# Performance work log

Hardware: AMD Instinct MI355X
Metric: run time of the kernel (lower is better)

Reference implementation:

```python
import jax, jax.numpy as jnp
import numpy as np

B, T, C, H = 2, 1024, 768, 12
D = C // H
HID = 4 * C
EPS_YAT = 1e-6
EPS_LN = 1e-6


def yat_dense(x, kernel, bias, alpha):
    # scale = (sqrt(n_out)/log(1+n_out))**alpha
    y = x @ kernel
    dist = (jnp.sum(x * x, axis=-1, keepdims=True)
            + jnp.sum(kernel * kernel, axis=0) - 2.0 * y)
    y = (y * y) / (dist + EPS_YAT)
    if bias is not None:
        y = y + bias
    n = kernel.shape[1]
    scale = (jnp.sqrt(jnp.float32(n)) / jnp.log1p(jnp.float32(n))) ** alpha
    return y * scale


def layernorm(x, scale):
    mu = jnp.mean(x, axis=-1, keepdims=True)
    var = jnp.mean((x - mu) ** 2, axis=-1, keepdims=True)
    return (x - mu) * jax.lax.rsqrt(var + EPS_LN) * scale


def rope_table(seq_len, dim):
    freqs = jnp.exp(jnp.arange(0, dim, 2, dtype=jnp.float32)
                    * (-jnp.log(10000.0) / dim))
    angles = jnp.arange(seq_len, dtype=jnp.float32)[:, None] * freqs[None, :]
    return jnp.concatenate([jnp.cos(angles), jnp.sin(angles)], axis=-1)  # [T, D]


def block_forward(x, mask, p):
    Bc, Tc, Cc = x.shape
    h = layernorm(x, p['ln1_scale'])
    qkv = yat_dense(h, p['w_qkv'], p['b_qkv'], p['a_qkv'])  # [B,T,3C]
    qkv = qkv.reshape(Bc, Tc, 3, H, D)
    q, k, v = qkv[:, :, 0], qkv[:, :, 1], qkv[:, :, 2]      # [B,T,H,D]
    rope = rope_table(Tc, D)[:, None, :]                     # [T,1,D]
    q = q * rope
    k = k * rope
    scale = 1.0 / jnp.sqrt(jnp.float32(D))
    attn = jnp.einsum('bihd,bjhd->bhij', q, k) * scale       # [B,H,T,T]
    attn = jnp.where(mask, attn, jnp.finfo(attn.dtype).min)
    attn = jax.nn.softmax(attn, axis=-1)
    o = jnp.einsum('bhij,bjhd->bihd', attn, v).reshape(Bc, Tc, Cc)
    o = yat_dense(o, p['w_ao'], p['b_ao'], p['a_ao'])
    x = x + o
    h = layernorm(x, p['ln2_scale'])
    gate = yat_dense(h, p['w_fc'], p['b_fc'], p['a_fc'])
    u = yat_dense(h, p['w_gate'], p['b_gate'], p['a_gate'])
    u = jax.nn.gelu(u) * gate
    u = yat_dense(u, p['w_proj'], p['b_proj'], p['a_proj'])
    return x + u


def setup_inputs() -> dict:
    key = jax.random.key(0)
    ks = jax.random.split(key, 8)
    x = jax.random.normal(ks[0], (B, T, C), dtype=jnp.float32)
    mask = jnp.tril(jnp.ones((T, T), dtype=bool))[None, None]  # causal [1,1,T,T]
    w = lambda k, shp: 0.02 * jax.random.normal(k, shp, dtype=jnp.float32)
    return {
        'x': x, 'mask': mask,
        'ln1_scale': jnp.ones((C,), jnp.float32),
        'w_qkv': w(ks[1], (C, 3 * C)), 'b_qkv': jnp.zeros((3 * C,), jnp.float32),
        'a_qkv': jnp.ones((1,), jnp.float32),
        'w_ao': w(ks[2], (C, C)), 'b_ao': jnp.zeros((C,), jnp.float32),
        'a_ao': jnp.ones((1,), jnp.float32),
        'ln2_scale': jnp.ones((C,), jnp.float32),
        'w_fc': w(ks[3], (C, HID)), 'b_fc': jnp.zeros((HID,), jnp.float32),
        'a_fc': jnp.ones((1,), jnp.float32),
        'w_gate': w(ks[4], (C, HID)), 'b_gate': jnp.zeros((HID,), jnp.float32),
        'a_gate': jnp.ones((1,), jnp.float32),
        'w_proj': w(ks[5], (HID, C)), 'b_proj': jnp.zeros((C,), jnp.float32),
        'a_proj': jnp.ones((1,), jnp.float32),
    }


def reference(x, mask, ln1_scale, w_qkv, b_qkv, a_qkv, w_ao, b_ao, a_ao,
              ln2_scale, w_fc, b_fc, a_fc, w_gate, b_gate, a_gate,
              w_proj, b_proj, a_proj):
    p = dict(ln1_scale=ln1_scale, w_qkv=w_qkv, b_qkv=b_qkv, a_qkv=a_qkv,
             w_ao=w_ao, b_ao=b_ao, a_ao=a_ao, ln2_scale=ln2_scale,
             w_fc=w_fc, b_fc=b_fc, a_fc=a_fc, w_gate=w_gate, b_gate=b_gate,
             a_gate=a_gate, w_proj=w_proj, b_proj=b_proj, a_proj=a_proj)
    return block_forward(x, mask, p)
```

## Files before the change

### kernel.cpp

```cpp
#include <hip/hip_runtime.h>
#include <cstdint>

#define DEVFN static __device__ __forceinline__

typedef __bf16 bf16x8 __attribute__((ext_vector_type(8)));
typedef float f32x4 __attribute__((ext_vector_type(4)));
typedef float f32x16 __attribute__((ext_vector_type(16)));
typedef unsigned short us4 __attribute__((ext_vector_type(4)));

DEVFN unsigned short f2bf(float f) {
  unsigned u = __float_as_uint(f);
  u += 0x7fffu + ((u >> 16) & 1u);
  return (unsigned short)(u >> 16);
}
DEVFN float bf2f(unsigned short h) { return __uint_as_float(((unsigned)h) << 16); }
DEVFN void async16(const void* g, void* l) {
  __builtin_amdgcn_global_load_lds((__attribute__((address_space(1))) const void*)g,
                                   (__attribute__((address_space(3))) void*)l, 16, 0, 0);
}
DEVFN float gelu_t(float u) {
  float z = 0.7978845608028654f * (u + 0.044715f * u * u * u);
  float zc = fminf(fmaxf(z, -15.f), 15.f);
  float e = __expf(2.f * zc);
  return u * __fdividef(e, e + 1.f);
}
DEVFN int xcd_swizzle(int lin, int total) {
  return (lin & 7) * (total >> 3) + (lin >> 3);
}
DEVFN int row32(int r, int lhalf) { return (r & 3) + 8 * (r >> 2) + 4 * lhalf; }

struct PrepArgs {
  float* rope;
  const float* W[5]; unsigned short* Wt[5]; float* cn[5];
  int N[5]; int off[6];
  const float* x; const float* g1s; unsigned short* h1; float* hrow1;
};
__global__ __launch_bounds__(256) void k_prep(PrepArgs a) {
  __shared__ float tile[32][33];
  __shared__ float part[8][32];
  __shared__ float red[12];
  const int bid = blockIdx.x, tid = threadIdx.x;
  if (bid < 256) {
    int g = bid * 256 + tid;
    int t = g >> 6, dd = g & 63, i = dd & 31;
    float fr = __expf(-0.2878231366242558f * (float)i);
    float ang = (float)t * fr;
    a.rope[g] = (dd < 32) ? cosf(ang) : sinf(ang);
  } else if (bid < 9472) {
    int lin = bid - 256;
    int e = 0;
    while (lin >= a.off[e + 1]) ++e;
    int local = lin - a.off[e];
    const int N = a.N[e];
    int nbx = N >> 5;
    int tn = local % nbx, tk = local / nbx;
    const float* W = a.W[e];
    unsigned short* Wt = a.Wt[e];
    float* cn = a.cn[e];
    const int K = (e == 4) ? 3072 : 768;
    int tx = tid & 31, ty = tid >> 5;
    float acc = 0.f;
    #pragma unroll
    for (int j = 0; j < 4; ++j) {
      int r = ty + j * 8;
      float v = W[(long)(tk * 32 + r) * N + tn * 32 + tx];
      tile[r][tx] = v;
      acc += v * v;
    }
    part[ty][tx] = acc;
    __syncthreads();
    #pragma unroll
    for (int j = 0; j < 4; ++j) {
      int rr = ty + j * 8;
      Wt[(long)(tn * 32 + rr) * K + tk * 32 + tx] = f2bf(tile[tx][rr]);
    }
    if (ty == 0) {
      float s = part[0][tx];
      #pragma unroll
      for (int jj = 1; jj < 8; ++jj) s += part[jj][tx];
      atomicAdd(&cn[tn * 32 + tx], s);
    }
  } else {
    int row = bid - 9472;
    const float* xr = a.x + (long)row * 768;
    float v0 = xr[tid], v1 = xr[tid + 256], v2 = xr[tid + 512];
    float s = v0 + v1 + v2;
    float ss = v0 * v0 + v1 * v1 + v2 * v2;
    #pragma unroll
    for (int o = 32; o; o >>= 1) { s += __shfl_xor(s, o); ss += __shfl_xor(ss, o); }
    int wv = tid >> 6;
    if ((tid & 63) == 0) { red[wv] = s; red[wv + 4] = ss; }
    __syncthreads();
    s = red[0] + red[1] + red[2] + red[3];
    ss = red[4] + red[5] + red[6] + red[7];
    float mu = s * (1.f / 768.f);
    float var = ss * (1.f / 768.f) - mu * mu;
    float rs = rsqrtf(var + 1e-6f);
    float h0 = (v0 - mu) * rs * a.g1s[tid];
    float h1 = (v1 - mu) * rs * a.g1s[tid + 256];
    float h2 = (v2 - mu) * rs * a.g1s[tid + 512];
    unsigned short* hr = a.h1 + (long)row * 768;
    hr[tid] = f2bf(h0); hr[tid + 256] = f2bf(h1); hr[tid + 512] = f2bf(h2);
    float p = h0 * h0 + h1 * h1 + h2 * h2;
    #pragma unroll
    for (int o = 32; o; o >>= 1) p += __shfl_xor(p, o);
    if ((tid & 63) == 0) red[8 + wv] = p;
    __syncthreads();
    if (tid == 0) a.hrow1[row] = red[8] + red[9] + red[10] + red[11];
  }
}

__global__ __launch_bounds__(256) void k_ln(const float* __restrict__ x,
    const float* __restrict__ g, unsigned short* __restrict__ h, float* __restrict__ row2) {
  int row = blockIdx.x, tid = threadIdx.x;
  const float* xr = x + (long)row * 768;
  float v0 = xr[tid], v1 = xr[tid + 256], v2 = xr[tid + 512];
  float s = v0 + v1 + v2;
  float ss = v0 * v0 + v1 * v1 + v2 * v2;
  #pragma unroll
  for (int o = 32; o; o >>= 1) { s += __shfl_xor(s, o); ss += __shfl_xor(ss, o); }
  __shared__ float red[12];
  int wv = tid >> 6;
  if ((tid & 63) == 0) { red[wv] = s; red[wv + 4] = ss; }
  __syncthreads();
  s = red[0] + red[1] + red[2] + red[3];
  ss = red[4] + red[5] + red[6] + red[7];
  float mu = s * (1.f / 768.f);
  float var = ss * (1.f / 768.f) - mu * mu;
  float rs = rsqrtf(var + 1e-6f);
  float h0 = (v0 - mu) * rs * g[tid];
  float h1 = (v1 - mu) * rs * g[tid + 256];
  float h2 = (v2 - mu) * rs * g[tid + 512];
  unsigned short* hr = h + (long)row * 768;
  hr[tid] = f2bf(h0); hr[tid + 256] = f2bf(h1); hr[tid + 512] = f2bf(h2);
  float p = h0 * h0 + h1 * h1 + h2 * h2;
  #pragma unroll
  for (int o = 32; o; o >>= 1) p += __shfl_xor(p, o);
  if ((tid & 63) == 0) red[8 + wv] = p;
  __syncthreads();
  if (tid == 0) row2[row] = red[8] + red[9] + red[10] + red[11];
}

constexpr int M_QKV = 0, M_AO = 1;

struct GemmArgs {
  const unsigned short* A; const unsigned short* Bt;
  const float* arow2; const float* wcol2; const float* bias; const float* alpha;
  int N; int ks;
  const float* rope;
  unsigned short* qo; unsigned short* ko; unsigned short* vo;
  const float* xf; float* xo;
};

template <int MODE, int NI, int NBM, int NBN>
__global__ __launch_bounds__(256, 4) void k_gemm(GemmArgs p) {
  __shared__ __align__(16) unsigned short As[3][2048];
  __shared__ __align__(16) unsigned short Bs[3][4096];
  const int tid = threadIdx.x, wave = tid >> 6, lane = tid & 63;
  const int quad = lane >> 4, l = lane & 15;
  constexpr int TOTAL = NBM * NBN;
  const int g = xcd_swizzle(blockIdx.x, TOTAL);
  const int bm = (g % NBM) * 64;
  const int bn = (g / NBM) * 128;
  const int ks = p.ks;
  const int wm = (wave & 1) * 32, wn = (wave >> 1) * 64;
  const f32x4 fzero = {0.f, 0.f, 0.f, 0.f};
  f32x4 acc[2][4];
  #pragma unroll
  for (int i = 0; i < 2; ++i)
    #pragma unroll
    for (int j = 0; j < 4; ++j) acc[i][j] = fzero;
  const int sw = (l >> 1) & 3;

  auto stage = [&](int s, int k0) {
    {
      int ci = tid;
      int r = ci >> 2;
      int c = (ci & 3) ^ ((r >> 1) & 3);
      async16(p.A + (long)(bm + r) * ks + k0 + c * 8, &As[s][ci * 8]);
    }
    #pragma unroll
    for (int it = 0; it < 2; ++it) {
      int ci = tid + it * 256;
      int r = ci >> 2;
      int c = (ci & 3) ^ ((r >> 1) & 3);
      async16(p.Bt + (long)(bn + r) * ks + k0 + c * 8, &Bs[s][ci * 8]);
    }
  };
  auto compute = [&](int s) {
    bf16x8 af[2], bfv[4];
    #pragma unroll
    for (int mi = 0; mi < 2; ++mi)
      af[mi] = *(const bf16x8*)&As[s][(wm + mi * 16 + l) * 32 + ((quad ^ sw) * 8)];
    #pragma unroll
    for (int ni = 0; ni < 4; ++ni)
      bfv[ni] = *(const bf16x8*)&Bs[s][(wn + ni * 16 + l) * 32 + ((quad ^ sw) * 8)];
    #pragma unroll
    for (int mi = 0; mi < 2; ++mi)
      #pragma unroll
      for (int ni = 0; ni < 4; ++ni)
        acc[mi][ni] = __builtin_amdgcn_mfma_f32_16x16x32_bf16(af[mi], bfv[ni], acc[mi][ni], 0, 0, 0);
  };
  auto iter = [&](int s, int i) {
    if (i + 1 >= NI) { asm volatile("s_waitcnt vmcnt(0)" ::: "memory"); }
    else             { asm volatile("s_waitcnt vmcnt(3)" ::: "memory"); }
    __builtin_amdgcn_s_barrier();
    asm volatile("" ::: "memory");
    if (i + 2 < NI) stage(s == 0 ? 2 : s - 1, (i + 2) * 32);
    compute(s);
  };

  stage(0, 0);
  stage(1, 32);
  int i = 0;
  while (i < NI) {
    iter(0, i); ++i;
    iter(1, i); ++i;
    iter(2, i); ++i;
  }

  const float al = p.alpha[0];
  const float nn = (float)p.N;
  const float ys = powf(sqrtf(nn) / log1pf(nn), al);
  #pragma unroll
  for (int ni = 0; ni < 4; ++ni) {
    const int j = bn + wn + ni * 16 + l;
    const float w2 = p.wcol2[j];
    const float bj = p.bias[j];
    int s3 = 0, hh = 0, dd = 0;
    if constexpr (MODE == M_QKV) { s3 = j / 768; int rem = j - s3 * 768; hh = rem >> 6; dd = rem & 63; }
    #pragma unroll
    for (int mi = 0; mi < 2; ++mi) {
      const int i0 = bm + wm + mi * 16 + quad * 4;
      float vv[4];
      #pragma unroll
      for (int rg = 0; rg < 4; ++rg) {
        const float y = acc[mi][ni][rg];
        const float dist = p.arow2[i0 + rg] + w2 - 2.f * y + 1e-6f;
        vv[rg] = (__fdividef(y * y, dist) + bj) * ys;
      }
      if constexpr (MODE == M_QKV) {
        int b = i0 >> 10, t0 = i0 & 1023;
        if (s3 == 2) {
          us4 pk = {f2bf(vv[0]), f2bf(vv[1]), f2bf(vv[2]), f2bf(vv[3])};
          *(us4*)&p.vo[((long)(b * 12 + hh) * 64 + dd) * 1024 + t0] = pk;
        } else {
          unsigned short* dst = (s3 == 0) ? p.qo : p.ko;
          #pragma unroll
          for (int rg = 0; rg < 4; ++rg) {
            float ro = p.rope[(t0 + rg) * 64 + dd];
            dst[((long)(b * 12 + hh) * 1024 + t0 + rg) * 64 + dd] = f2bf(vv[rg] * ro);
          }
        }
      } else {
        #pragma unroll
        for (int rg = 0; rg < 4; ++rg) {
          long idx = (long)(i0 + rg) * 768 + j;
          p.xo[idx] = p.xf[idx] + vv[rg];
        }
      }
    }
  }
}


struct PartArgs {
  const unsigned short* A; const unsigned short* Bt;
  unsigned short* partb;
};
__global__ __launch_bounds__(256, 3) void k_part32(PartArgs p) {
  constexpr int NI = 12, KS = 3072;
  __shared__ __align__(16) unsigned short As[3][4096];
  __shared__ __align__(16) unsigned short Bs[3][4096];
  const int tid = threadIdx.x, wave = tid >> 6, lane = tid & 63;
  const int l5 = lane >> 5, l31 = lane & 31;
  const int g = xcd_swizzle(blockIdx.x, 768);
  const int bm = (g % 16) * 128;
  const int rest = g / 16;
  const int bn = (rest % 6) * 128;
  const int z = rest / 6;
  const int kb = z * 384;
  const int wm = (wave & 1) * 64, wn = (wave >> 1) * 64;
  f32x16 acc[2][2];
  #pragma unroll
  for (int i = 0; i < 2; ++i)
    #pragma unroll
    for (int j = 0; j < 2; ++j)
      #pragma unroll
      for (int c = 0; c < 16; ++c) acc[i][j][c] = 0.f;

  auto stage = [&](int s, int k0) {
    #pragma unroll
    for (int it = 0; it < 2; ++it) {
      int ci = tid + it * 256;
      int r = ci >> 2;
      int c = (ci & 3) ^ (r & 3);
      async16(p.A + (long)(bm + r) * KS + kb + k0 + c * 8, &As[s][ci * 8]);
      async16(p.Bt + (long)(bn + r) * KS + kb + k0 + c * 8, &Bs[s][ci * 8]);
    }
  };
  auto compute = [&](int s) {
    #pragma unroll
    for (int kh = 0; kh < 2; ++kh) {
      bf16x8 a[2], b[2];
      #pragma unroll
      for (int mi = 0; mi < 2; ++mi) {
        int r = wm + mi * 32 + l31;
        a[mi] = *(const bf16x8*)&As[s][r * 32 + (((kh * 2 + l5) ^ (r & 3)) * 8)];
      }
      #pragma unroll
      for (int ni = 0; ni < 2; ++ni) {
        int r = wn + ni * 32 + l31;
        b[ni] = *(const bf16x8*)&Bs[s][r * 32 + (((kh * 2 + l5) ^ (r & 3)) * 8)];
      }
      #pragma unroll
      for (int mi = 0; mi < 2; ++mi)
        #pragma unroll
        for (int ni = 0; ni < 2; ++ni)
          acc[mi][ni] = __builtin_amdgcn_mfma_f32_32x32x16_bf16(a[mi], b[ni], acc[mi][ni], 0, 0, 0);
    }
  };
  auto iter = [&](int s, int i) {
    if (i + 1 >= NI) { asm volatile("s_waitcnt vmcnt(0)" ::: "memory"); }
    else             { asm volatile("s_waitcnt vmcnt(4)" ::: "memory"); }
    __builtin_amdgcn_s_barrier();
    asm volatile("" ::: "memory");
    if (i + 2 < NI) stage(s == 0 ? 2 : s - 1, (i + 2) * 32);
    compute(s);
  };

  stage(0, 0);
  stage(1, 32);
  int i = 0;
  while (i < NI) {
    iter(0, i); ++i;
    iter(1, i); ++i;
    iter(2, i); ++i;
  }

  unsigned short* slab = p.partb + (long)z * (2048 * 768);
  #pragma unroll
  for (int mi = 0; mi < 2; ++mi)
    #pragma unroll
    for (int ni = 0; ni < 2; ++ni) {
      const int j = bn + wn + ni * 32 + l31;
      #pragma unroll
      for (int rg = 0; rg < 16; ++rg) {
        const int ii = bm + wm + mi * 32 + row32(rg, l5);
        slab[(long)ii * 768 + j] = f2bf(acc[mi][ni][rg]);
      }
    }
}

struct MlpArgs {
  const unsigned short* A; const unsigned short* Bf; const unsigned short* Bg;
  const float* arow2; const float* w2f; const float* w2g;
  const float* bf; const float* bg; const float* af_; const float* ag_;
  unsigned short* mlp; float* mrow2;
};
__global__ __launch_bounds__(256, 2) void k_mlp32(MlpArgs p) {
  constexpr int NI = 24, K = 768;
  __shared__ __align__(16) unsigned short As[3][4096];
  __shared__ __align__(16) unsigned short Bfs[3][4096];
  __shared__ __align__(16) unsigned short Bgs[3][4096];
  const int tid = threadIdx.x, wave = tid >> 6, lane = tid & 63;
  const int l5 = lane >> 5, l31 = lane & 31;
  const int g = xcd_swizzle(blockIdx.x, 384);
  const int bm = (g % 16) * 128, bn = (g / 16) * 128;
  const int wm = (wave & 1) * 64, wn = (wave >> 1) * 64;
  f32x16 accf[2][2], accg[2][2];
  #pragma unroll
  for (int i = 0; i < 2; ++i)
    #pragma unroll
    for (int j = 0; j < 2; ++j)
      #pragma unroll
      for (int c = 0; c < 16; ++c) { accf[i][j][c] = 0.f; accg[i][j][c] = 0.f; }

  auto stage = [&](int s, int k0) {
    #pragma unroll
    for (int it = 0; it < 2; ++it) {
      int ci = tid + it * 256;
      int r = ci >> 2;
      int c = (ci & 3) ^ (r & 3);
      async16(p.A  + (long)(bm + r) * K + k0 + c * 8, &As[s][ci * 8]);
      async16(p.Bf + (long)(bn + r) * K + k0 + c * 8, &Bfs[s][ci * 8]);
      async16(p.Bg + (long)(bn + r) * K + k0 + c * 8, &Bgs[s][ci * 8]);
    }
  };
  auto compute = [&](int s) {
    #pragma unroll
    for (int kh = 0; kh < 2; ++kh) {
      bf16x8 a[2], bfv[2], bgv[2];
      #pragma unroll
      for (int mi = 0; mi < 2; ++mi) {
        int r = wm + mi * 32 + l31;
        a[mi] = *(const bf16x8*)&As[s][r * 32 + (((kh * 2 + l5) ^ (r & 3)) * 8)];
      }
      #pragma unroll
      for (int ni = 0; ni < 2; ++ni) {
        int r = wn + ni * 32 + l31;
        int off = r * 32 + (((kh * 2 + l5) ^ (r & 3)) * 8);
        bfv[ni] = *(const bf16x8*)&Bfs[s][off];
        bgv[ni] = *(const bf16x8*)&Bgs[s][off];
      }
      #pragma unroll
      for (int mi = 0; mi < 2; ++mi)
        #pragma unroll
        for (int ni = 0; ni < 2; ++ni) {
          accf[mi][ni] = __builtin_amdgcn_mfma_f32_32x32x16_bf16(a[mi], bfv[ni], accf[mi][ni], 0, 0, 0);
          accg[mi][ni] = __builtin_amdgcn_mfma_f32_32x32x16_bf16(a[mi], bgv[ni], accg[mi][ni], 0, 0, 0);
        }
    }
  };
  auto iter = [&](int s, int i) {
    if (i + 1 >= NI) { asm volatile("s_waitcnt vmcnt(0)" ::: "memory"); }
    else             { asm volatile("s_waitcnt vmcnt(6)" ::: "memory"); }
    __builtin_amdgcn_s_barrier();
    asm volatile("" ::: "memory");
    if (i + 2 < NI) stage(s == 0 ? 2 : s - 1, (i + 2) * 32);
    compute(s);
  };

  stage(0, 0);
  stage(1, 32);
  int i = 0;
  while (i < NI) {
    iter(0, i); ++i;
    iter(1, i); ++i;
    iter(2, i); ++i;
  }

  const float ysf = powf(sqrtf(3072.f) / log1pf(3072.f), p.af_[0]);
  const float ysg = powf(sqrtf(3072.f) / log1pf(3072.f), p.ag_[0]);
  float w2f[2], w2g[2], bjf[2], bjg[2]; int js[2];
  #pragma unroll
  for (int ni = 0; ni < 2; ++ni) {
    int j = bn + wn + ni * 32 + l31;
    js[ni] = j; w2f[ni] = p.w2f[j]; w2g[ni] = p.w2g[j]; bjf[ni] = p.bf[j]; bjg[ni] = p.bg[j];
  }
  #pragma unroll
  for (int mi = 0; mi < 2; ++mi) {
    #pragma unroll
    for (int rg = 0; rg < 16; ++rg) {
      const int ii = bm + wm + mi * 32 + row32(rg, l5);
      const float a2 = p.arow2[ii];
      float rsum = 0.f;
      #pragma unroll
      for (int ni = 0; ni < 2; ++ni) {
        float yf = accf[mi][ni][rg];
        float gate = (__fdividef(yf * yf, a2 + w2f[ni] - 2.f * yf + 1e-6f) + bjf[ni]) * ysf;
        float yg = accg[mi][ni][rg];
        float u  = (__fdividef(yg * yg, a2 + w2g[ni] - 2.f * yg + 1e-6f) + bjg[ni]) * ysg;
        float out = gelu_t(u) * gate;
        p.mlp[(long)ii * 3072 + js[ni]] = f2bf(out);
        rsum += out * out;
      }
      #pragma unroll
      for (int o = 16; o; o >>= 1) rsum += __shfl_xor(rsum, o);
      if (l31 == 0) atomicAdd(&p.mrow2[ii], rsum);
    }
  }
}

struct EpiArgs {
  const unsigned short* slab; const float* arow2; const float* wcol2;
  const float* bias; const float* alpha; const float* xo; float* outf;
};
__global__ __launch_bounds__(256) void k_proj_epi(EpiArgs p) {
  int g = blockIdx.x * 256 + threadIdx.x;
  int i = g / 192, jv = (g - i * 192) * 4;
  long base = (long)i * 768 + jv;
  f32x4 y = {0.f, 0.f, 0.f, 0.f};
  #pragma unroll
  for (int z = 0; z < 8; ++z) {
    us4 s4 = *(const us4*)(p.slab + (long)z * 1572864 + base);
    #pragma unroll
    for (int c = 0; c < 4; ++c) y[c] += bf2f(s4[c]);
  }
  const float a2 = p.arow2[i];
  const float ys = powf(sqrtf(768.f) / log1pf(768.f), p.alpha[0]);
  f32x4 xo4 = *(const f32x4*)(p.xo + base);
  f32x4 out;
  #pragma unroll
  for (int c = 0; c < 4; ++c) {
    float yy = y[c];
    float dist = a2 + p.wcol2[jv + c] - 2.f * yy + 1e-6f;
    out[c] = xo4[c] + (__fdividef(yy * yy, dist) + p.bias[jv + c]) * ys;
  }
  *(f32x4*)(p.outf + base) = out;
}

__global__ __launch_bounds__(256) void k_attn(const unsigned short* __restrict__ qb,
    const unsigned short* __restrict__ kb, const unsigned short* __restrict__ vb,
    unsigned short* __restrict__ ob, float* __restrict__ orow2) {
  __shared__ __align__(16) unsigned short Qs[4096];
  __shared__ __align__(16) unsigned short Ks[3][4096];
  __shared__ __align__(16) unsigned short Vs[3][4096];
  __shared__ __align__(16) unsigned short Ps[4096];
  const int tid = threadIdx.x, wave = tid >> 6, lane = tid & 63;
  const int quad = lane >> 4, l = lane & 15;
  const int g = xcd_swizzle(blockIdx.x, 16 * 24);
  const int bh = g % 24, qt = 15 - (g / 24);
  const int b = bh / 12, hh = bh % 12;
  const int q0 = qt * 64;
  const f32x4 fzero = {0.f, 0.f, 0.f, 0.f};

  auto stage_kv = [&](int s, int jt) {
    const unsigned short* kg = kb + ((long)bh * 1024 + jt * 64) * 64;
    const unsigned short* vg = vb + (long)bh * 64 * 1024 + jt * 64;
    #pragma unroll
    for (int it = 0; it < 2; ++it) {
      int ci = tid + it * 256;
      int r = ci >> 3;
      int c = (ci & 7) ^ (r & 7);
      async16(kg + (long)r * 64 + c * 8, &Ks[s][ci * 8]);
      async16(vg + (long)r * 1024 + c * 8, &Vs[s][ci * 8]);
    }
  };

  const unsigned short* qg = qb + ((long)bh * 1024 + q0) * 64;
  #pragma unroll
  for (int it = 0; it < 2; ++it) {
    int ci = tid + it * 256;
    int r = ci >> 3;
    int c = (ci & 7) ^ (r & 7);
    async16(qg + (long)r * 64 + c * 8, &Qs[ci * 8]);
  }
  stage_kv(0, 0);
  if (qt >= 1) {
    stage_kv(1, 1);
    asm volatile("s_waitcnt vmcnt(4)" ::: "memory");
  } else {
    asm volatile("s_waitcnt vmcnt(0)" ::: "memory");
  }
  __builtin_amdgcn_s_barrier();
  asm volatile("" ::: "memory");

  bf16x8 aq[2];
  #pragma unroll
  for (int ks = 0; ks < 2; ++ks)
    aq[ks] = *(const bf16x8*)&Qs[(wave * 16 + l) * 64 + (((ks * 4 + quad) ^ (l & 7)) * 8)];

  f32x4 O[4];
  float mi_[4], li[4];
  #pragma unroll
  for (int f = 0; f < 4; ++f) O[f] = fzero;
  #pragma unroll
  for (int r = 0; r < 4; ++r) { mi_[r] = -1e30f; li[r] = 0.f; }

  for (int jt = 0; jt <= qt; ++jt) {
    const int s = jt % 3;
    if (jt > 0) {
      if (jt + 1 <= qt) { asm volatile("s_waitcnt vmcnt(4)" ::: "memory"); }
      else              { asm volatile("s_waitcnt vmcnt(0)" ::: "memory"); }
      __builtin_amdgcn_s_barrier();
      asm volatile("" ::: "memory");
    }
    if (jt + 2 <= qt) stage_kv((jt + 2) % 3, jt + 2);

    f32x4 S[4];
    #pragma unroll
    for (int f = 0; f < 4; ++f) S[f] = fzero;
    #pragma unroll
    for (int ks = 0; ks < 2; ++ks) {
      #pragma unroll
      for (int f = 0; f < 4; ++f) {
        bf16x8 bk = *(const bf16x8*)&Ks[s][(f * 16 + l) * 64 + (((ks * 4 + quad) ^ (l & 7)) * 8)];
        S[f] = __builtin_amdgcn_mfma_f32_16x16x32_bf16(aq[ks], bk, S[f], 0, 0, 0);
      }
    }
    const bool diag = (jt == qt);
    #pragma unroll
    for (int f = 0; f < 4; ++f)
      #pragma unroll
      for (int r = 0; r < 4; ++r) {
        float v = S[f][r] * 0.125f;
        if (diag && (f * 16 + l > wave * 16 + quad * 4 + r)) v = -1e30f;
        S[f][r] = v;
      }
    #pragma unroll
    for (int r = 0; r < 4; ++r) {
      float mx = fmaxf(fmaxf(S[0][r], S[1][r]), fmaxf(S[2][r], S[3][r]));
      #pragma unroll
      for (int o = 8; o; o >>= 1) mx = fmaxf(mx, __shfl_xor(mx, o));
      float mnew = fmaxf(mi_[r], mx);
      float alr = __expf(mi_[r] - mnew);
      float sum = 0.f;
      #pragma unroll
      for (int f = 0; f < 4; ++f) {
        float e = __expf(S[f][r] - mnew);
        S[f][r] = e;
        sum += e;
      }
      #pragma unroll
      for (int o = 8; o; o >>= 1) sum += __shfl_xor(sum, o);
      li[r] = li[r] * alr + sum;
      #pragma unroll
      for (int f = 0; f < 4; ++f) O[f][r] *= alr;
      mi_[r] = mnew;
    }
    #pragma unroll
    for (int f = 0; f < 4; ++f)
      #pragma unroll
      for (int r = 0; r < 4; ++r) {
        int i = quad * 4 + r;
        int j = f * 16 + l;
        int pch = (j >> 3) ^ (i & 7);
        Ps[wave * 1024 + i * 64 + pch * 8 + (j & 7)] = f2bf(S[f][r]);
      }
    #pragma unroll
    for (int ks = 0; ks < 2; ++ks) {
      bf16x8 ap = *(const bf16x8*)&Ps[wave * 1024 + l * 64 + (((ks * 4 + quad) ^ (l & 7)) * 8)];
      #pragma unroll
      for (int f = 0; f < 4; ++f) {
        bf16x8 bv = *(const bf16x8*)&Vs[s][(f * 16 + l) * 64 + (((ks * 4 + quad) ^ (l & 7)) * 8)];
        O[f] = __builtin_amdgcn_mfma_f32_16x16x32_bf16(ap, bv, O[f], 0, 0, 0);
      }
    }
  }
  float inv[4];
  #pragma unroll
  for (int r = 0; r < 4; ++r) inv[r] = __fdividef(1.f, li[r]);
  #pragma unroll
  for (int f = 0; f < 4; ++f)
    #pragma unroll
    for (int r = 0; r < 4; ++r) {
      int t = q0 + wave * 16 + quad * 4 + r;
      int dd = f * 16 + l;
      ob[((long)(b * 1024 + t) * 12 + hh) * 64 + dd] = f2bf(O[f][r] * inv[r]);
    }
  #pragma unroll
  for (int r = 0; r < 4; ++r) {
    float rsum = 0.f;
    #pragma unroll
    for (int f = 0; f < 4; ++f) { float v = O[f][r] * inv[r]; rsum += v * v; }
    #pragma unroll
    for (int o = 8; o; o >>= 1) rsum += __shfl_xor(rsum, o);
    if (l == 0) {
      int t = q0 + wave * 16 + quad * 4 + r;
      atomicAdd(&orow2[b * 1024 + t], rsum);
    }
  }
}

extern "C" void kernel_launch(void* const* d_in, const int* in_sizes, int n_in,
                              void* d_out, int out_size, void* d_ws, size_t ws_size,
                              hipStream_t stream) {
  (void)in_sizes; (void)n_in; (void)out_size;
  char* w = (char*)d_ws;
  size_t off = 0;
  auto alloc = [&](size_t bytes) -> void* {
    void* p = w + off;
    off = (off + bytes + 255) & ~(size_t)255;
    return p;
  };
  float* rope            = (float*)alloc(65536 * 4);
  unsigned short* wtqkv  = (unsigned short*)alloc((size_t)2304 * 768 * 2);
  unsigned short* wtao   = (unsigned short*)alloc((size_t)768 * 768 * 2);
  unsigned short* wtfc   = (unsigned short*)alloc((size_t)3072 * 768 * 2);
  unsigned short* wtgate = (unsigned short*)alloc((size_t)3072 * 768 * 2);
  unsigned short* wtproj = (unsigned short*)alloc((size_t)768 * 3072 * 2);
  float* zeroed          = (float*)alloc(14080 * 4);
  unsigned short* h1     = (unsigned short*)alloc((size_t)2048 * 768 * 2);
  float* hrow1           = (float*)alloc(2048 * 4);
  unsigned short* qbuf   = (unsigned short*)alloc((size_t)2048 * 768 * 2);
  unsigned short* kbuf   = (unsigned short*)alloc((size_t)2048 * 768 * 2);
  unsigned short* vbuf   = (unsigned short*)alloc((size_t)2048 * 768 * 2);
  unsigned short* obuf   = (unsigned short*)alloc((size_t)2048 * 768 * 2);
  float* xo              = (float*)alloc((size_t)2048 * 768 * 4);
  unsigned short* h2     = (unsigned short*)alloc((size_t)2048 * 768 * 2);
  float* hrow2           = (float*)alloc(2048 * 4);
  unsigned short* mlp    = (unsigned short*)alloc((size_t)2048 * 3072 * 2);
  unsigned short* slabs  = (unsigned short*)alloc((size_t)8 * 2048 * 768 * 2);
  if (off > ws_size) return;

  float* wcol2  = zeroed;
  float* orow2  = zeroed + 9984;
  float* mrow2  = zeroed + 9984 + 2048;
  float* c_qkv  = wcol2 + 0;
  float* c_ao   = wcol2 + 2304;
  float* c_fc   = wcol2 + 3072;
  float* c_gate = wcol2 + 6144;
  float* c_proj = wcol2 + 9216;

  const float* xin = (const float*)d_in[0];

  hipMemsetAsync(zeroed, 0, 14080 * 4, stream);

  PrepArgs pa;
  pa.rope = rope;
  pa.W[0] = (const float*)d_in[3];  pa.Wt[0] = wtqkv;  pa.cn[0] = c_qkv;  pa.N[0] = 2304;
  pa.W[1] = (const float*)d_in[6];  pa.Wt[1] = wtao;   pa.cn[1] = c_ao;   pa.N[1] = 768;
  pa.W[2] = (const float*)d_in[10]; pa.Wt[2] = wtfc;   pa.cn[2] = c_fc;   pa.N[2] = 3072;
  pa.W[3] = (const float*)d_in[13]; pa.Wt[3] = wtgate; pa.cn[3] = c_gate; pa.N[3] = 3072;
  pa.W[4] = (const float*)d_in[16]; pa.Wt[4] = wtproj; pa.cn[4] = c_proj; pa.N[4] = 768;
  pa.off[0] = 0; pa.off[1] = 1728; pa.off[2] = 2304; pa.off[3] = 4608;
  pa.off[4] = 6912; pa.off[5] = 9216;
  pa.x = xin; pa.g1s = (const float*)d_in[2]; pa.h1 = h1; pa.hrow1 = hrow1;
  k_prep<<<11520, 256, 0, stream>>>(pa);

  GemmArgs gq = {};
  gq.A = h1; gq.Bt = wtqkv; gq.arow2 = hrow1; gq.wcol2 = c_qkv;
  gq.bias = (const float*)d_in[4]; gq.alpha = (const float*)d_in[5];
  gq.N = 2304; gq.ks = 768;
  gq.rope = rope; gq.qo = qbuf; gq.ko = kbuf; gq.vo = vbuf;
  k_gemm<M_QKV, 24, 32, 18><<<576, 256, 0, stream>>>(gq);

  k_attn<<<384, 256, 0, stream>>>(qbuf, kbuf, vbuf, obuf, orow2);

  GemmArgs ga = {};
  ga.A = obuf; ga.Bt = wtao; ga.arow2 = orow2; ga.wcol2 = c_ao;
  ga.bias = (const float*)d_in[7]; ga.alpha = (const float*)d_in[8];
  ga.N = 768; ga.ks = 768;
  ga.xf = xin; ga.xo = xo;
  k_gemm<M_AO, 24, 32, 6><<<192, 256, 0, stream>>>(ga);

  k_ln<<<2048, 256, 0, stream>>>(xo, (const float*)d_in[9], h2, hrow2);

  MlpArgs gm = {};
  gm.A = h2; gm.Bf = wtfc; gm.Bg = wtgate; gm.arow2 = hrow2;
  gm.w2f = c_fc; gm.w2g = c_gate;
  gm.bf = (const float*)d_in[11]; gm.bg = (const float*)d_in[14];
  gm.af_ = (const float*)d_in[12]; gm.ag_ = (const float*)d_in[15];
  gm.mlp = mlp; gm.mrow2 = mrow2;
  k_mlp32<<<384, 256, 0, stream>>>(gm);

  PartArgs gp = {};
  gp.A = mlp; gp.Bt = wtproj; gp.partb = slabs;
  k_part32<<<768, 256, 0, stream>>>(gp);

  EpiArgs ge = {};
  ge.slab = slabs; ge.arow2 = mrow2; ge.wcol2 = c_proj;
  ge.bias = (const float*)d_in[17]; ge.alpha = (const float*)d_in[18];
  ge.xo = xo; ge.outf = (float*)d_out;
  k_proj_epi<<<1536, 256, 0, stream>>>(ge);
}
```

Baseline: 285.8 us.

## Shrink M tiles, use fragment-ordered LDS, load A directly in MLP GEMM

```diff
diff --git a/kernel.cpp b/kernel.cpp
--- a/kernel.cpp
+++ b/kernel.cpp
@@ -268,61 +268,56 @@
   const unsigned short* A; const unsigned short* Bt;
   unsigned short* partb;
 };
-__global__ __launch_bounds__(256, 3) void k_part32(PartArgs p) {
-  constexpr int NI = 12, KS = 3072;
-  __shared__ __align__(16) unsigned short As[3][4096];
+__global__ __launch_bounds__(256, 4) void k_part32(PartArgs p) {
+  constexpr int NI = 24, KS = 3072;
+  __shared__ __align__(16) unsigned short As[3][2048];
   __shared__ __align__(16) unsigned short Bs[3][4096];
   const int tid = threadIdx.x, wave = tid >> 6, lane = tid & 63;
   const int l5 = lane >> 5, l31 = lane & 31;
   const int g = xcd_swizzle(blockIdx.x, 768);
-  const int bm = (g % 16) * 128;
-  const int rest = g / 16;
+  const int bm = (g % 32) * 64;
+  const int rest = g / 32;
   const int bn = (rest % 6) * 128;
   const int z = rest / 6;
-  const int kb = z * 384;
-  const int wm = (wave & 1) * 64, wn = (wave >> 1) * 64;
-  f32x16 acc[2][2];
-  #pragma unroll
-  for (int i = 0; i < 2; ++i)
-    #pragma unroll
-    for (int j = 0; j < 2; ++j)
-      #pragma unroll
-      for (int c = 0; c < 16; ++c) acc[i][j][c] = 0.f;
+  const int kb = z * 768;
+  const int wm = (wave & 1) * 32, wn = (wave >> 1) * 64;
+  f32x16 acc[2];
+  #pragma unroll
+  for (int j = 0; j < 2; ++j)
+    #pragma unroll
+    for (int c = 0; c < 16; ++c) acc[j][c] = 0.f;
 
   auto stage = [&](int s, int k0) {
+    {
+      int ci = tid;
+      int G = ci >> 7, kh = (ci >> 6) & 1, cl = (ci >> 5) & 1, r31 = ci & 31;
+      async16(p.A + (long)(bm + G * 32 + r31) * KS + kb + k0 + (kh * 2 + cl) * 8,
+              &As[s][ci * 8]);
+    }
     #pragma unroll
     for (int it = 0; it < 2; ++it) {
       int ci = tid + it * 256;
-      int r = ci >> 2;
-      int c = (ci & 3) ^ (r & 3);
-      async16(p.A + (long)(bm + r) * KS + kb + k0 + c * 8, &As[s][ci * 8]);
-      async16(p.Bt + (long)(bn + r) * KS + kb + k0 + c * 8, &Bs[s][ci * 8]);
+      int G = ci >> 7, kh = (ci >> 6) & 1, cl = (ci >> 5) & 1, r31 = ci & 31;
+      async16(p.Bt + (long)(bn + G * 32 + r31) * KS + kb + k0 + (kh * 2 + cl) * 8,
+              &Bs[s][ci * 8]);
     }
   };
   auto compute = [&](int s) {
+    const int Ga = (wave & 1);
+    const int Gn0 = (wave >> 1) * 2;
     #pragma unroll
     for (int kh = 0; kh < 2; ++kh) {
-      bf16x8 a[2], b[2];
-      #pragma unroll
-      for (int mi = 0; mi < 2; ++mi) {
-        int r = wm + mi * 32 + l31;
-        a[mi] = *(const bf16x8*)&As[s][r * 32 + (((kh * 2 + l5) ^ (r & 3)) * 8)];
-      }
+      bf16x8 a = *(const bf16x8*)&As[s][(Ga * 128 + kh * 64 + lane) * 8];
       #pragma unroll
       for (int ni = 0; ni < 2; ++ni) {
-        int r = wn + ni * 32 + l31;
-        b[ni] = *(const bf16x8*)&Bs[s][r * 32 + (((kh * 2 + l5) ^ (r & 3)) * 8)];
-      }
-      #pragma unroll
-      for (int mi = 0; mi < 2; ++mi)
-        #pragma unroll
-        for (int ni = 0; ni < 2; ++ni)
-          acc[mi][ni] = __builtin_amdgcn_mfma_f32_32x32x16_bf16(a[mi], b[ni], acc[mi][ni], 0, 0, 0);
+        bf16x8 b = *(const bf16x8*)&Bs[s][((Gn0 + ni) * 128 + kh * 64 + lane) * 8];
+        acc[ni] = __builtin_amdgcn_mfma_f32_32x32x16_bf16(a, b, acc[ni], 0, 0, 0);
+      }
     }
   };
   auto iter = [&](int s, int i) {
     if (i + 1 >= NI) { asm volatile("s_waitcnt vmcnt(0)" ::: "memory"); }
-    else             { asm volatile("s_waitcnt vmcnt(4)" ::: "memory"); }
+    else             { asm volatile("s_waitcnt vmcnt(3)" ::: "memory"); }
     __builtin_amdgcn_s_barrier();
     asm volatile("" ::: "memory");
     if (i + 2 < NI) stage(s == 0 ? 2 : s - 1, (i + 2) * 32);
@@ -340,16 +335,14 @@
 
   unsigned short* slab = p.partb + (long)z * (2048 * 768);
   #pragma unroll
-  for (int mi = 0; mi < 2; ++mi)
-    #pragma unroll
-    for (int ni = 0; ni < 2; ++ni) {
-      const int j = bn + wn + ni * 32 + l31;
-      #pragma unroll
-      for (int rg = 0; rg < 16; ++rg) {
-        const int ii = bm + wm + mi * 32 + row32(rg, l5);
-        slab[(long)ii * 768 + j] = f2bf(acc[mi][ni][rg]);
-      }
-    }
+  for (int ni = 0; ni < 2; ++ni) {
+    const int j = bn + wn + ni * 32 + l31;
+    #pragma unroll
+    for (int rg = 0; rg < 16; ++rg) {
+      const int ii = bm + wm + row32(rg, l5);
+      slab[(long)ii * 768 + j] = f2bf(acc[ni][rg]);
+    }
+  }
 }
 
 struct MlpArgs {
@@ -358,76 +351,58 @@
   const float* bf; const float* bg; const float* af_; const float* ag_;
   unsigned short* mlp; float* mrow2;
 };
-__global__ __launch_bounds__(256, 2) void k_mlp32(MlpArgs p) {
+__global__ __launch_bounds__(256, 3) void k_mlp32(MlpArgs p) {
   constexpr int NI = 24, K = 768;
-  __shared__ __align__(16) unsigned short As[3][4096];
   __shared__ __align__(16) unsigned short Bfs[3][4096];
   __shared__ __align__(16) unsigned short Bgs[3][4096];
   const int tid = threadIdx.x, wave = tid >> 6, lane = tid & 63;
   const int l5 = lane >> 5, l31 = lane & 31;
-  const int g = xcd_swizzle(blockIdx.x, 384);
-  const int bm = (g % 16) * 128, bn = (g / 16) * 128;
-  const int wm = (wave & 1) * 64, wn = (wave >> 1) * 64;
-  f32x16 accf[2][2], accg[2][2];
-  #pragma unroll
-  for (int i = 0; i < 2; ++i)
-    #pragma unroll
-    for (int j = 0; j < 2; ++j)
-      #pragma unroll
-      for (int c = 0; c < 16; ++c) { accf[i][j][c] = 0.f; accg[i][j][c] = 0.f; }
-
-  auto stage = [&](int s, int k0) {
+  const int g = xcd_swizzle(blockIdx.x, 768);
+  const int bm = (g % 32) * 64, bn = (g / 32) * 128;
+  const int wm = (wave & 1) * 32, wn = (wave >> 1) * 64;
+  f32x16 accf[2], accg[2];
+  #pragma unroll
+  for (int j = 0; j < 2; ++j)
+    #pragma unroll
+    for (int c = 0; c < 16; ++c) { accf[j][c] = 0.f; accg[j][c] = 0.f; }
+
+  auto stageB = [&](int s, int k0) {
     #pragma unroll
     for (int it = 0; it < 2; ++it) {
       int ci = tid + it * 256;
-      int r = ci >> 2;
-      int c = (ci & 3) ^ (r & 3);
-      async16(p.A  + (long)(bm + r) * K + k0 + c * 8, &As[s][ci * 8]);
-      async16(p.Bf + (long)(bn + r) * K + k0 + c * 8, &Bfs[s][ci * 8]);
-      async16(p.Bg + (long)(bn + r) * K + k0 + c * 8, &Bgs[s][ci * 8]);
-    }
-  };
-  auto compute = [&](int s) {
-    #pragma unroll
-    for (int kh = 0; kh < 2; ++kh) {
-      bf16x8 a[2], bfv[2], bgv[2];
-      #pragma unroll
-      for (int mi = 0; mi < 2; ++mi) {
-        int r = wm + mi * 32 + l31;
-        a[mi] = *(const bf16x8*)&As[s][r * 32 + (((kh * 2 + l5) ^ (r & 3)) * 8)];
-      }
-      #pragma unroll
-      for (int ni = 0; ni < 2; ++ni) {
-        int r = wn + ni * 32 + l31;
-        int off = r * 32 + (((kh * 2 + l5) ^ (r & 3)) * 8);
-        bfv[ni] = *(const bf16x8*)&Bfs[s][off];
-        bgv[ni] = *(const bf16x8*)&Bgs[s][off];
-      }
-      #pragma unroll
-      for (int mi = 0; mi < 2; ++mi)
-        #pragma unroll
-        for (int ni = 0; ni < 2; ++ni) {
-          accf[mi][ni] = __builtin_amdgcn_mfma_f32_32x32x16_bf16(a[mi], bfv[ni], accf[mi][ni], 0, 0, 0);
-          accg[mi][ni] = __builtin_amdgcn_mfma_f32_32x32x16_bf16(a[mi], bgv[ni], accg[mi][ni], 0, 0, 0);
-        }
-    }
-  };
-  auto iter = [&](int s, int i) {
-    if (i + 1 >= NI) { asm volatile("s_waitcnt vmcnt(0)" ::: "memory"); }
+      int G = ci >> 7, kh = (ci >> 6) & 1, cl = (ci >> 5) & 1, r31 = ci & 31;
+      long ro = (long)(bn + G * 32 + r31) * K + k0 + (kh * 2 + cl) * 8;
+      async16(p.Bf + ro, &Bfs[s][ci * 8]);
+      async16(p.Bg + ro, &Bgs[s][ci * 8]);
+    }
+  };
+
+  stageB(0, 0);
+  stageB(1, 32);
+  const unsigned short* Arow = p.A + (long)(bm + wm + l31) * K + l5 * 8;
+  const int Gn0 = (wave >> 1) * 2;
+  for (int i = 0; i < NI; ++i) {
+    const int s = i % 3;
+    const int k0 = i * 32;
+    bf16x8 af0 = *(const bf16x8*)(Arow + k0);
+    bf16x8 af1 = *(const bf16x8*)(Arow + k0 + 16);
+    if (i + 1 >= NI) { asm volatile("s_waitcnt vmcnt(2)" ::: "memory"); }
     else             { asm volatile("s_waitcnt vmcnt(6)" ::: "memory"); }
     __builtin_amdgcn_s_barrier();
     asm volatile("" ::: "memory");
-    if (i + 2 < NI) stage(s == 0 ? 2 : s - 1, (i + 2) * 32);
-    compute(s);
-  };
-
-  stage(0, 0);
-  stage(1, 32);
-  int i = 0;
-  while (i < NI) {
-    iter(0, i); ++i;
-    iter(1, i); ++i;
-    iter(2, i); ++i;
+    if (i + 2 < NI) stageB((i + 2) % 3, (i + 2) * 32);
+    #pragma unroll
+    for (int kh = 0; kh < 2; ++kh) {
+      bf16x8 a = (kh == 0) ? af0 : af1;
+      #pragma unroll
+      for (int ni = 0; ni < 2; ++ni) {
+        int slot = (Gn0 + ni) * 128 + kh * 64 + lane;
+        bf16x8 bf_ = *(const bf16x8*)&Bfs[s][slot * 8];
+        bf16x8 bg_ = *(const bf16x8*)&Bgs[s][slot * 8];
+        accf[ni] = __builtin_amdgcn_mfma_f32_32x32x16_bf16(a, bf_, accf[ni], 0, 0, 0);
+        accg[ni] = __builtin_amdgcn_mfma_f32_32x32x16_bf16(a, bg_, accg[ni], 0, 0, 0);
+      }
+    }
   }
 
   const float ysf = powf(sqrtf(3072.f) / log1pf(3072.f), p.af_[0]);
@@ -439,26 +414,23 @@
     js[ni] = j; w2f[ni] = p.w2f[j]; w2g[ni] = p.w2g[j]; bjf[ni] = p.bf[j]; bjg[ni] = p.bg[j];
   }
   #pragma unroll
-  for (int mi = 0; mi < 2; ++mi) {
-    #pragma unroll
-    for (int rg = 0; rg < 16; ++rg) {
-      const int ii = bm + wm + mi * 32 + row32(rg, l5);
-      const float a2 = p.arow2[ii];
-      float rsum = 0.f;
-      #pragma unroll
-      for (int ni = 0; ni < 2; ++ni) {
-        float yf = accf[mi][ni][rg];
-        float gate = (__fdividef(yf * yf, a2 + w2f[ni] - 2.f * yf + 1e-6f) + bjf[ni]) * ysf;
-        float yg = accg[mi][ni][rg];
-        float u  = (__fdividef(yg * yg, a2 + w2g[ni] - 2.f * yg + 1e-6f) + bjg[ni]) * ysg;
-        float out = gelu_t(u) * gate;
-        p.mlp[(long)ii * 3072 + js[ni]] = f2bf(out);
-        rsum += out * out;
-      }
-      #pragma unroll
-      for (int o = 16; o; o >>= 1) rsum += __shfl_xor(rsum, o);
-      if (l31 == 0) atomicAdd(&p.mrow2[ii], rsum);
-    }
+  for (int rg = 0; rg < 16; ++rg) {
+    const int ii = bm + wm + row32(rg, l5);
+    const float a2 = p.arow2[ii];
+    float rsum = 0.f;
+    #pragma unroll
+    for (int ni = 0; ni < 2; ++ni) {
+      float yf = accf[ni][rg];
+      float gate = (__fdividef(yf * yf, a2 + w2f[ni] - 2.f * yf + 1e-6f) + bjf[ni]) * ysf;
+      float yg = accg[ni][rg];
+      float u  = (__fdividef(yg * yg, a2 + w2g[ni] - 2.f * yg + 1e-6f) + bjg[ni]) * ysg;
+      float out = gelu_t(u) * gate;
+      p.mlp[(long)ii * 3072 + js[ni]] = f2bf(out);
+      rsum += out * out;
+    }
+    #pragma unroll
+    for (int o = 16; o; o >>= 1) rsum += __shfl_xor(rsum, o);
+    if (l31 == 0) atomicAdd(&p.mrow2[ii], rsum);
   }
 }
 
@@ -472,7 +444,7 @@
   long base = (long)i * 768 + jv;
   f32x4 y = {0.f, 0.f, 0.f, 0.f};
   #pragma unroll
-  for (int z = 0; z < 8; ++z) {
+  for (int z = 0; z < 4; ++z) {
     us4 s4 = *(const us4*)(p.slab + (long)z * 1572864 + base);
     #pragma unroll
     for (int c = 0; c < 4; ++c) y[c] += bf2f(s4[c]);
@@ -671,7 +643,7 @@
   unsigned short* h2     = (unsigned short*)alloc((size_t)2048 * 768 * 2);
   float* hrow2           = (float*)alloc(2048 * 4);
   unsigned short* mlp    = (unsigned short*)alloc((size_t)2048 * 3072 * 2);
-  unsigned short* slabs  = (unsigned short*)alloc((size_t)8 * 2048 * 768 * 2);
+  unsigned short* slabs  = (unsigned short*)alloc((size_t)4 * 2048 * 768 * 2);
   if (off > ws_size) return;
 
   float* wcol2  = zeroed;
@@ -723,7 +695,7 @@
   gm.bf = (const float*)d_in[11]; gm.bg = (const float*)d_in[14];
   gm.af_ = (const float*)d_in[12]; gm.ag_ = (const float*)d_in[15];
   gm.mlp = mlp; gm.mrow2 = mrow2;
-  k_mlp32<<<384, 256, 0, stream>>>(gm);
+  k_mlp32<<<768, 256, 0, stream>>>(gm);
 
   PartArgs gp = {};
   gp.A = mlp; gp.Bt = wtproj; gp.partb = slabs;
```

New measurement: 304.6 us. 6.6% more time.

## Enlarge MLP and proj GEMM tiles to 256x128 with BK=64 double buffering

Applied to the files above, without the earlier changes.

```diff
diff --git a/kernel.cpp b/kernel.cpp
--- a/kernel.cpp
+++ b/kernel.cpp
@@ -28,6 +28,7 @@
   return (lin & 7) * (total >> 3) + (lin >> 3);
 }
 DEVFN int row32(int r, int lhalf) { return (r & 3) + 8 * (r >> 2) + 4 * lhalf; }
+
 
 struct PrepArgs {
   float* rope;
@@ -264,113 +265,25 @@
 }
 
 
-struct PartArgs {
-  const unsigned short* A; const unsigned short* Bt;
-  unsigned short* partb;
-};
-__global__ __launch_bounds__(256, 3) void k_part32(PartArgs p) {
-  constexpr int NI = 12, KS = 3072;
-  __shared__ __align__(16) unsigned short As[3][4096];
-  __shared__ __align__(16) unsigned short Bs[3][4096];
-  const int tid = threadIdx.x, wave = tid >> 6, lane = tid & 63;
-  const int l5 = lane >> 5, l31 = lane & 31;
-  const int g = xcd_swizzle(blockIdx.x, 768);
-  const int bm = (g % 16) * 128;
-  const int rest = g / 16;
-  const int bn = (rest % 6) * 128;
-  const int z = rest / 6;
-  const int kb = z * 384;
-  const int wm = (wave & 1) * 64, wn = (wave >> 1) * 64;
-  f32x16 acc[2][2];
-  #pragma unroll
-  for (int i = 0; i < 2; ++i)
-    #pragma unroll
-    for (int j = 0; j < 2; ++j)
-      #pragma unroll
-      for (int c = 0; c < 16; ++c) acc[i][j][c] = 0.f;
-
-  auto stage = [&](int s, int k0) {
-    #pragma unroll
-    for (int it = 0; it < 2; ++it) {
-      int ci = tid + it * 256;
-      int r = ci >> 2;
-      int c = (ci & 3) ^ (r & 3);
-      async16(p.A + (long)(bm + r) * KS + kb + k0 + c * 8, &As[s][ci * 8]);
-      async16(p.Bt + (long)(bn + r) * KS + kb + k0 + c * 8, &Bs[s][ci * 8]);
-    }
-  };
-  auto compute = [&](int s) {
-    #pragma unroll
-    for (int kh = 0; kh < 2; ++kh) {
-      bf16x8 a[2], b[2];
-      #pragma unroll
-      for (int mi = 0; mi < 2; ++mi) {
-        int r = wm + mi * 32 + l31;
-        a[mi] = *(const bf16x8*)&As[s][r * 32 + (((kh * 2 + l5) ^ (r & 3)) * 8)];
-      }
-      #pragma unroll
-      for (int ni = 0; ni < 2; ++ni) {
-        int r = wn + ni * 32 + l31;
-        b[ni] = *(const bf16x8*)&Bs[s][r * 32 + (((kh * 2 + l5) ^ (r & 3)) * 8)];
-      }
-      #pragma unroll
-      for (int mi = 0; mi < 2; ++mi)
-        #pragma unroll
-        for (int ni = 0; ni < 2; ++ni)
-          acc[mi][ni] = __builtin_amdgcn_mfma_f32_32x32x16_bf16(a[mi], b[ni], acc[mi][ni], 0, 0, 0);
-    }
-  };
-  auto iter = [&](int s, int i) {
-    if (i + 1 >= NI) { asm volatile("s_waitcnt vmcnt(0)" ::: "memory"); }
-    else             { asm volatile("s_waitcnt vmcnt(4)" ::: "memory"); }
-    __builtin_amdgcn_s_barrier();
-    asm volatile("" ::: "memory");
-    if (i + 2 < NI) stage(s == 0 ? 2 : s - 1, (i + 2) * 32);
-    compute(s);
-  };
-
-  stage(0, 0);
-  stage(1, 32);
-  int i = 0;
-  while (i < NI) {
-    iter(0, i); ++i;
-    iter(1, i); ++i;
-    iter(2, i); ++i;
-  }
-
-  unsigned short* slab = p.partb + (long)z * (2048 * 768);
-  #pragma unroll
-  for (int mi = 0; mi < 2; ++mi)
-    #pragma unroll
-    for (int ni = 0; ni < 2; ++ni) {
-      const int j = bn + wn + ni * 32 + l31;
-      #pragma unroll
-      for (int rg = 0; rg < 16; ++rg) {
-        const int ii = bm + wm + mi * 32 + row32(rg, l5);
-        slab[(long)ii * 768 + j] = f2bf(acc[mi][ni][rg]);
-      }
-    }
-}
-
 struct MlpArgs {
   const unsigned short* A; const unsigned short* Bf; const unsigned short* Bg;
   const float* arow2; const float* w2f; const float* w2g;
   const float* bf; const float* bg; const float* af_; const float* ag_;
   unsigned short* mlp; float* mrow2;
 };
-__global__ __launch_bounds__(256, 2) void k_mlp32(MlpArgs p) {
-  constexpr int NI = 24, K = 768;
-  __shared__ __align__(16) unsigned short As[3][4096];
-  __shared__ __align__(16) unsigned short Bfs[3][4096];
-  __shared__ __align__(16) unsigned short Bgs[3][4096];
+__global__ __launch_bounds__(256, 1) void k_mlp256(MlpArgs p) {
+  constexpr int NI = 12, K = 768;
+  __shared__ __align__(16) unsigned short As[2][16384];
+  __shared__ __align__(16) unsigned short Bfs[2][8192];
+  __shared__ __align__(16) unsigned short Bgs[2][8192];
   const int tid = threadIdx.x, wave = tid >> 6, lane = tid & 63;
   const int l5 = lane >> 5, l31 = lane & 31;
-  const int g = xcd_swizzle(blockIdx.x, 384);
-  const int bm = (g % 16) * 128, bn = (g / 16) * 128;
-  const int wm = (wave & 1) * 64, wn = (wave >> 1) * 64;
-  f32x16 accf[2][2], accg[2][2];
-  #pragma unroll
-  for (int i = 0; i < 2; ++i)
+  const int g = xcd_swizzle(blockIdx.x, 192);
+  const int bm = (g % 8) * 256, bn = (g / 8) * 128;
+  const int wm = (wave & 1) * 128, wn = (wave >> 1) * 64;
+  f32x16 accf[4][2], accg[4][2];
+  #pragma unroll
+  for (int i = 0; i < 4; ++i)
     #pragma unroll
     for (int j = 0; j < 2; ++j)
       #pragma unroll
@@ -378,56 +291,52 @@
 
   auto stage = [&](int s, int k0) {
     #pragma unroll
-    for (int it = 0; it < 2; ++it) {
+    for (int it = 0; it < 8; ++it) {
       int ci = tid + it * 256;
-      int r = ci >> 2;
-      int c = (ci & 3) ^ (r & 3);
-      async16(p.A  + (long)(bm + r) * K + k0 + c * 8, &As[s][ci * 8]);
-      async16(p.Bf + (long)(bn + r) * K + k0 + c * 8, &Bfs[s][ci * 8]);
-      async16(p.Bg + (long)(bn + r) * K + k0 + c * 8, &Bgs[s][ci * 8]);
+      int G = ci >> 8, r31 = (ci >> 3) & 31, ch = (ci & 7) ^ (r31 & 7);
+      async16(p.A + (long)(bm + G * 32 + r31) * K + k0 + ch * 8, &As[s][ci * 8]);
+    }
+    #pragma unroll
+    for (int it = 0; it < 4; ++it) {
+      int ci = tid + it * 256;
+      int G = ci >> 8, r31 = (ci >> 3) & 31, ch = (ci & 7) ^ (r31 & 7);
+      long ro = (long)(bn + G * 32 + r31) * K + k0 + ch * 8;
+      async16(p.Bf + ro, &Bfs[s][ci * 8]);
+      async16(p.Bg + ro, &Bgs[s][ci * 8]);
     }
   };
-  auto compute = [&](int s) {
-    #pragma unroll
-    for (int kh = 0; kh < 2; ++kh) {
-      bf16x8 a[2], bfv[2], bgv[2];
-      #pragma unroll
-      for (int mi = 0; mi < 2; ++mi) {
-        int r = wm + mi * 32 + l31;
-        a[mi] = *(const bf16x8*)&As[s][r * 32 + (((kh * 2 + l5) ^ (r & 3)) * 8)];
+
+  stage(0, 0);
+  for (int i = 0; i < NI; ++i) {
+    const int s = i & 1;
+    asm volatile("s_waitcnt vmcnt(0)" ::: "memory");
+    __builtin_amdgcn_s_barrier();
+    asm volatile("" ::: "memory");
+    if (i + 1 < NI) stage(s ^ 1, (i + 1) * 64);
+    #pragma unroll
+    for (int kh = 0; kh < 4; ++kh) {
+      const int rd = ((kh * 2 + l5) ^ (l31 & 7));
+      bf16x8 a[4], bfv[2], bgv[2];
+      #pragma unroll
+      for (int mi = 0; mi < 4; ++mi) {
+        int Ga = (wm >> 5) + mi;
+        a[mi] = *(const bf16x8*)&As[s][(Ga * 256 + l31 * 8 + rd) * 8];
       }
       #pragma unroll
       for (int ni = 0; ni < 2; ++ni) {
-        int r = wn + ni * 32 + l31;
-        int off = r * 32 + (((kh * 2 + l5) ^ (r & 3)) * 8);
-        bfv[ni] = *(const bf16x8*)&Bfs[s][off];
-        bgv[ni] = *(const bf16x8*)&Bgs[s][off];
-      }
-      #pragma unroll
-      for (int mi = 0; mi < 2; ++mi)
+        int Gb = (wn >> 5) + ni;
+        int slot = Gb * 256 + l31 * 8 + rd;
+        bfv[ni] = *(const bf16x8*)&Bfs[s][slot * 8];
+        bgv[ni] = *(const bf16x8*)&Bgs[s][slot * 8];
+      }
+      #pragma unroll
+      for (int mi = 0; mi < 4; ++mi)
         #pragma unroll
         for (int ni = 0; ni < 2; ++ni) {
           accf[mi][ni] = __builtin_amdgcn_mfma_f32_32x32x16_bf16(a[mi], bfv[ni], accf[mi][ni], 0, 0, 0);
           accg[mi][ni] = __builtin_amdgcn_mfma_f32_32x32x16_bf16(a[mi], bgv[ni], accg[mi][ni], 0, 0, 0);
         }
     }
-  };
-  auto iter = [&](int s, int i) {
-    if (i + 1 >= NI) { asm volatile("s_waitcnt vmcnt(0)" ::: "memory"); }
-    else             { asm volatile("s_waitcnt vmcnt(6)" ::: "memory"); }
-    __builtin_amdgcn_s_barrier();
-    asm volatile("" ::: "memory");
-    if (i + 2 < NI) stage(s == 0 ? 2 : s - 1, (i + 2) * 32);
-    compute(s);
-  };
-
-  stage(0, 0);
-  stage(1, 32);
-  int i = 0;
-  while (i < NI) {
-    iter(0, i); ++i;
-    iter(1, i); ++i;
-    iter(2, i); ++i;
   }
 
   const float ysf = powf(sqrtf(3072.f) / log1pf(3072.f), p.af_[0]);
@@ -439,7 +348,7 @@
     js[ni] = j; w2f[ni] = p.w2f[j]; w2g[ni] = p.w2g[j]; bjf[ni] = p.bf[j]; bjg[ni] = p.bg[j];
   }
   #pragma unroll
-  for (int mi = 0; mi < 2; ++mi) {
+  for (int mi = 0; mi < 4; ++mi) {
     #pragma unroll
     for (int rg = 0; rg < 16; ++rg) {
       const int ii = bm + wm + mi * 32 + row32(rg, l5);
@@ -460,6 +369,89 @@
       if (l31 == 0) atomicAdd(&p.mrow2[ii], rsum);
     }
   }
+}
+
+struct PartArgs {
+  const unsigned short* A; const unsigned short* Bt;
+  unsigned short* partb;
+};
+__global__ __launch_bounds__(256, 1) void k_part256(PartArgs p) {
+  constexpr int NI = 12, KS = 3072;
+  __shared__ __align__(16) unsigned short As[2][16384];
+  __shared__ __align__(16) unsigned short Bs[2][8192];
+  const int tid = threadIdx.x, wave = tid >> 6, lane = tid & 63;
+  const int l5 = lane >> 5, l31 = lane & 31;
+  const int g = xcd_swizzle(blockIdx.x, 192);
+  const int bm = (g % 8) * 256;
+  const int rest = g / 8;
+  const int bn = (rest % 6) * 128;
+  const int z = rest / 6;
+  const int kb = z * 768;
+  const int wm = (wave & 1) * 128, wn = (wave >> 1) * 64;
+  f32x16 acc[4][2];
+  #pragma unroll
+  for (int i = 0; i < 4; ++i)
+    #pragma unroll
+    for (int j = 0; j < 2; ++j)
+      #pragma unroll
+      for (int c = 0; c < 16; ++c) acc[i][j][c] = 0.f;
+
+  auto stage = [&](int s, int k0) {
+    #pragma unroll
+    for (int it = 0; it < 8; ++it) {
+      int ci = tid + it * 256;
+      int G = ci >> 8, r31 = (ci >> 3) & 31, ch = (ci & 7) ^ (r31 & 7);
+      async16(p.A + (long)(bm + G * 32 + r31) * KS + kb + k0 + ch * 8, &As[s][ci * 8]);
+    }
+    #pragma unroll
+    for (int it = 0; it < 4; ++it) {
+      int ci = tid + it * 256;
+      int G = ci >> 8, r31 = (ci >> 3) & 31, ch = (ci & 7) ^ (r31 & 7);
+      async16(p.Bt + (long)(bn + G * 32 + r31) * KS + kb + k0 + ch * 8, &Bs[s][ci * 8]);
+    }
+  };
+
+  stage(0, 0);
+  for (int i = 0; i < NI; ++i) {
+    const int s = i & 1;
+    asm volatile("s_waitcnt vmcnt(0)" ::: "memory");
+    __builtin_amdgcn_s_barrier();
+    asm volatile("" ::: "memory");
+    if (i + 1 < NI) stage(s ^ 1, (i + 1) * 64);
+    #pragma unroll
+    for (int kh = 0; kh < 4; ++kh) {
+      const int rd = ((kh * 2 + l5) ^ (l31 & 7));
+      bf16x8 a[4], b[2];
+      #pragma unroll
+      for (int mi = 0; mi < 4; ++mi) {
+        int Ga = (wm >> 5) + mi;
+        a[mi] = *(const bf16x8*)&As[s][(Ga * 256 + l31 * 8 + rd) * 8];
+      }
+      #pragma unroll
+      for (int ni = 0; ni < 2; ++ni) {
+        int Gb = (wn >> 5) + ni;
+        b[ni] = *(const bf16x8*)&Bs[s][(Gb * 256 + l31 * 8 + rd) * 8];
+      }
+      #pragma unroll
+      for (int mi = 0; mi < 4; ++mi)
+        #pragma unroll
+        for (int ni = 0; ni < 2; ++ni)
+          acc[mi][ni] = __builtin_amdgcn_mfma_f32_32x32x16_bf16(a[mi], b[ni], acc[mi][ni], 0, 0, 0);
+    }
+  }
+
+  unsigned short* slab = p.partb + (long)z * (2048 * 768);
+  #pragma unroll
+  for (int mi = 0; mi < 4; ++mi)
+    #pragma unroll
+    for (int ni = 0; ni < 2; ++ni) {
+      const int j = bn + wn + ni * 32 + l31;
+      #pragma unroll
+      for (int rg = 0; rg < 16; ++rg) {
+        const int ii = bm + wm + mi * 32 + row32(rg, l5);
+        slab[(long)ii * 768 + j] = f2bf(acc[mi][ni][rg]);
+      }
+    }
 }
 
 struct EpiArgs {
@@ -472,7 +464,7 @@
   long base = (long)i * 768 + jv;
   f32x4 y = {0.f, 0.f, 0.f, 0.f};
   #pragma unroll
-  for (int z = 0; z < 8; ++z) {
+  for (int z = 0; z < 4; ++z) {
     us4 s4 = *(const us4*)(p.slab + (long)z * 1572864 + base);
     #pragma unroll
     for (int c = 0; c < 4; ++c) y[c] += bf2f(s4[c]);
@@ -671,7 +663,7 @@
   unsigned short* h2     = (unsigned short*)alloc((size_t)2048 * 768 * 2);
   float* hrow2           = (float*)alloc(2048 * 4);
   unsigned short* mlp    = (unsigned short*)alloc((size_t)2048 * 3072 * 2);
-  unsigned short* slabs  = (unsigned short*)alloc((size_t)8 * 2048 * 768 * 2);
+  unsigned short* slabs  = (unsigned short*)alloc((size_t)4 * 2048 * 768 * 2);
   if (off > ws_size) return;
 
   float* wcol2  = zeroed;
@@ -723,11 +715,11 @@
   gm.bf = (const float*)d_in[11]; gm.bg = (const float*)d_in[14];
   gm.af_ = (const float*)d_in[12]; gm.ag_ = (const float*)d_in[15];
   gm.mlp = mlp; gm.mrow2 = mrow2;
-  k_mlp32<<<384, 256, 0, stream>>>(gm);
+  k_mlp256<<<192, 256, 0, stream>>>(gm);
 
   PartArgs gp = {};
   gp.A = mlp; gp.Bt = wtproj; gp.partb = slabs;
-  k_part32<<<768, 256, 0, stream>>>(gp);
+  k_part256<<<192, 256, 0, stream>>>(gp);
 
   EpiArgs ge = {};
   ge.slab = slabs; ge.arow2 = mrow2; ge.wcol2 = c_proj;
```

After: 309.6 us. 8.3% more time.
